# Kernel tuning notes

Measured on AMD Instinct MI355X. Metric: run time of the kernel, lower is better.

The kernel has to match this reference:

```python
import jax, jax.numpy as jnp
import numpy as np

# norse.LIFCell default parameters
DT = 1e-3
TAU_SYN_INV = 200.0   # 1 / 5e-3
TAU_MEM_INV = 100.0   # 1 / 1e-2
V_TH = 1.0
V_LEAK = 0.0
V_RESET = 0.0
ALPHA = 100.0         # SuperSpike surrogate slope

T, B, N_IN, N_HIDDEN, N_OUT = 16, 4096, 784, 256, 10


@jax.custom_vjp
def heaviside(x):
    return (x > 0).astype(x.dtype)

def _h_fwd(x):
    return heaviside(x), x

def _h_bwd(x, g):
    # SuperSpike surrogate: d/dx H(x) ~ 1 / (alpha*|x| + 1)^2
    return (g / (ALPHA * jnp.abs(x) + 1.0) ** 2,)

heaviside.defvjp(_h_fwd, _h_bwd)


def lif_step(inp, v, i):
    """One norse lif_step: Euler-integrate v and i, spike, hard reset."""
    v_decayed = v + DT * TAU_MEM_INV * ((V_LEAK - v) + i)
    i_decayed = i - DT * TAU_SYN_INV * i
    z = heaviside(v_decayed - V_TH)
    v_new = (1.0 - z) * v_decayed + z * V_RESET
    i_new = i_decayed + inp
    return z, v_new, i_new


def setup_inputs() -> dict:
    key = jax.random.key(0)
    k1, k2, k3, k4, k5 = jax.random.split(key, 5)
    # binary spike trains (T, B, N_IN)
    spike_input = (jax.random.uniform(k1, (T, B, N_IN)) < 0.3).astype(jnp.float32)
    lim1 = float(1.0 / np.sqrt(N_IN))
    lim2 = float(1.0 / np.sqrt(N_HIDDEN))
    W1 = jax.random.uniform(k2, (N_HIDDEN, N_IN), minval=-lim1, maxval=lim1, dtype=jnp.float32)
    b1 = jax.random.uniform(k3, (N_HIDDEN,), minval=-lim1, maxval=lim1, dtype=jnp.float32)
    W2 = jax.random.uniform(k4, (N_OUT, N_HIDDEN), minval=-lim2, maxval=lim2, dtype=jnp.float32)
    b2 = jax.random.uniform(k5, (N_OUT,), minval=-lim2, maxval=lim2, dtype=jnp.float32)
    return {"spike_input": spike_input, "W1": W1, "b1": b1, "W2": W2, "b2": b2}


def reference(spike_input, W1, b1, W2, b2):
    batch = spike_input.shape[1]
    nh, no = W1.shape[0], W2.shape[0]
    dtype = spike_input.dtype
    # LIFCell with state=None starts at v=v_leak, i=0
    init = (jnp.full((batch, nh), V_LEAK, dtype), jnp.zeros((batch, nh), dtype),
            jnp.full((batch, no), V_LEAK, dtype), jnp.zeros((batch, no), dtype))

    def step(carry, x_t):
        v1, i1, v2, i2 = carry
        c1 = x_t @ W1.T + b1                 # (B, N_HIDDEN)
        z1, v1, i1 = lif_step(c1, v1, i1)
        c2 = z1 @ W2.T + b2                  # (B, N_OUT)
        z2, v2, i2 = lif_step(c2, v2, i2)
        return (v1, i1, v2, i2), z2

    _, zs = jax.lax.scan(step, init, spike_input)  # zs: (T, B, N_OUT)
    return zs.sum(axis=0)                          # (B, N_OUT)
```

## Files before the change

kernel.cpp:

```cpp
#include <hip/hip_runtime.h>


#define T_STEPS 16
#define B_SZ    4096
#define N_IN    784
#define N_HID   256
#define N_OUT   10
#define M_TOT   (T_STEPS * B_SZ)
#define KP8     832
#define NSTEP   13
#define WPLANE  (N_HID * KP8)

typedef int    i32x4 __attribute__((ext_vector_type(4)));
typedef unsigned int u32;
typedef unsigned char u8;

#define GLOAD_LDS(SRC, DST) \
    __builtin_amdgcn_global_load_lds( \
        (const __attribute__((address_space(1))) void*)(SRC), \
        (__attribute__((address_space(3))) void*)(DST), 16, 0, 0)

__global__ __launch_bounds__(256) void conv_x(
    const float* __restrict__ X, u8* __restrict__ Xq)
{
    const long idx = (long)blockIdx.x * 256 + threadIdx.x;
    const long m = idx / 52;
    const int  s = (int)(idx - m * 52);
    uint4 o = make_uint4(0u, 0u, 0u, 0u);
    if (s < 49) {
        const uint4* src = reinterpret_cast<const uint4*>(X + m * N_IN + s * 16);
        const uint4 f0 = src[0], f1 = src[1], f2 = src[2], f3 = src[3];
        auto pk = [](uint4 f) -> u32 {
            return (f.x ? 1u : 0u) | ((f.y ? 1u : 0u) << 8) |
                   ((f.z ? 1u : 0u) << 16) | ((f.w ? 1u : 0u) << 24);
        };
        o.x = pk(f0); o.y = pk(f1); o.z = pk(f2); o.w = pk(f3);
    }
    reinterpret_cast<uint4*>(Xq)[idx] = o;
}

__global__ __launch_bounds__(256) void conv_w3(
    const float* __restrict__ W1, char* __restrict__ Wq)
{
    const int idx = blockIdx.x * 256 + threadIdx.x;
    if (idx >= N_HID * KP8) return;
    const int n = idx / KP8, k = idx % KP8;
    const float w = (k < N_IN) ? W1[n * N_IN + k] : 0.0f;
    const float a = rintf(w * 2048.0f);
    const float r1 = fmaf(a, -4.8828125e-4f, w);
    const float b = rintf(r1 * 262144.0f);
    const float r2 = fmaf(b, -3.814697265625e-6f, r1);
    const float c = rintf(r2 * 33554432.0f);
    Wq[idx]              = (char)(int)a;
    Wq[WPLANE + idx]     = (char)(int)b;
    Wq[2 * WPLANE + idx] = (char)(int)c;
}

__global__ __launch_bounds__(256, 2) void gemm1_i8(
    const u8* __restrict__ Xq,
    const u8* __restrict__ Wq,
    const float* __restrict__ b1,
    float* __restrict__ C)
{
    __shared__ u8 Bq[3 * 32 * KP8];

    const int tid  = threadIdx.x;
    const int lane = tid & 63;
    const int w    = tid >> 6;
    const int bid = blockIdx.x;
    const int mt  = (bid & 7) | ((bid >> 6) << 3);
    const int ns  = (bid >> 3) & 7;
    const int m0  = mt * 256;
    const int n0  = ns * 32;
    const int ls  = lane >> 4;
    const int lr  = lane & 15;

    {
        const int nIt = (w < 2) ? 20 : 19;
        for (int it = 0; it < nIt; ++it) {
            const int u     = it * 256 + tid;
            const int plane = u / 1664;
            const int rem   = u - plane * 1664;
            const int row   = rem / 52;
            const int sp    = rem - row * 52;
            const int sl    = (sp & ~3) | ((sp & 3) ^ (row & 3));
            const u8* src = Wq + (size_t)plane * WPLANE +
                            (size_t)(n0 + row) * KP8 + sl * 16;
            GLOAD_LDS(src, &Bq[u * 16]);
        }
    }
    __syncthreads();

    const u8* aP[4];
    #pragma unroll
    for (int i = 0; i < 4; ++i)
        aP[i] = Xq + (size_t)(m0 + w * 64 + i * 16 + lr) * KP8 + ls * 16;

    int bOff[2][3];
    #pragma unroll
    for (int j = 0; j < 2; ++j) {
        const int row = j * 16 + lr;
        #pragma unroll
        for (int p = 0; p < 3; ++p)
            bOff[j][p] = p * (32 * KP8) + row * KP8 + ((ls ^ (row & 3)) << 4);
    }

    i32x4 acc[4][2][3];
    #pragma unroll
    for (int i = 0; i < 4; ++i)
        #pragma unroll
        for (int j = 0; j < 2; ++j)
            #pragma unroll
            for (int p = 0; p < 3; ++p)
                acc[i][j][p] = (i32x4){0, 0, 0, 0};

    auto mmstep = [&](const uint4* af, int s) {
        uint4 bf[2][3];
        #pragma unroll
        for (int j = 0; j < 2; ++j)
            #pragma unroll
            for (int p = 0; p < 3; ++p)
                bf[j][p] = *reinterpret_cast<const uint4*>(&Bq[bOff[j][p] + s * 64]);
        #pragma unroll
        for (int i = 0; i < 4; ++i)
            #pragma unroll
            for (int j = 0; j < 2; ++j)
                #pragma unroll
                for (int p = 0; p < 3; ++p)
                    acc[i][j][p] = __builtin_amdgcn_mfma_i32_16x16x64_i8(
                        __builtin_bit_cast(i32x4, af[i]),
                        __builtin_bit_cast(i32x4, bf[j][p]),
                        acc[i][j][p], 0, 0, 0);
    };

    uint4 afA[4], afB[4];
    #pragma unroll
    for (int i = 0; i < 4; ++i)
        afA[i] = *reinterpret_cast<const uint4*>(aP[i]);

    for (int s = 0; s < 12; s += 2) {
        #pragma unroll
        for (int i = 0; i < 4; ++i)
            afB[i] = *reinterpret_cast<const uint4*>(aP[i] + (s + 1) * 64);
        mmstep(afA, s);
        #pragma unroll
        for (int i = 0; i < 4; ++i)
            afA[i] = *reinterpret_cast<const uint4*>(aP[i] + (s + 2) * 64);
        mmstep(afB, s + 1);
    }
    mmstep(afA, 12);

    const float s1 = 4.8828125e-4f;
    const float s2 = 3.814697265625e-6f;
    const float s3 = 2.9802322387695312e-8f;
    #pragma unroll
    for (int j = 0; j < 2; ++j) {
        const int col  = n0 + j * 16 + lr;
        const float bb = b1[col];
        #pragma unroll
        for (int i = 0; i < 4; ++i) {
            const int rbase = m0 + w * 64 + i * 16 + (ls << 2);
            #pragma unroll
            for (int q = 0; q < 4; ++q) {
                const float v = fmaf(s1, (float)acc[i][j][0][q],
                                fmaf(s2, (float)acc[i][j][1][q],
                                fmaf(s3, (float)acc[i][j][2][q], bb)));
                C[(size_t)(rbase + q) * N_HID + col] = v;
            }
        }
    }
}

__global__ __launch_bounds__(256) void lif1_kernel(float* __restrict__ C1)
{
    const int g = blockIdx.x * 256 + threadIdx.x;
    const size_t stride = (size_t)B_SZ * N_HID;
    float v = 0.0f, cur = 0.0f;
    #pragma unroll
    for (int t = 0; t < T_STEPS; ++t) {
        const size_t off = (size_t)t * stride + g;
        const float c = C1[off];
        const float vd = v + 0.1f * ((0.0f - v) + cur);
        const float id = cur - 0.2f * cur;
        const bool  sp = vd > 1.0f;
        C1[off] = sp ? 1.0f : 0.0f;
        v = sp ? 0.0f : vd;
        cur = id + c;
    }
}

__global__ __launch_bounds__(640) void gemm2_f32(
    const float* __restrict__ Z, const float* __restrict__ W2,
    const float* __restrict__ b2, float* __restrict__ C2)
{
    __shared__ float zs[64 * 268];
    __shared__ float ws[N_OUT * N_HID];
    const int tid = threadIdx.x;
    const int m0 = blockIdx.x * 64;

    for (int idx = tid; idx < 4096; idx += 640) {
        const int r = idx >> 6;
        const int c = (idx & 63) << 2;
        *(float4*)&zs[r * 268 + c] =
            *(const float4*)&Z[(size_t)(m0 + r) * N_HID + c];
    }
    *(float4*)&ws[tid * 4] = *(const float4*)&W2[tid * 4];
    __syncthreads();

    const int o = tid >> 6;
    const int r = tid & 63;
    float acc = b2[o];
    #pragma unroll
    for (int k = 0; k < N_HID; k += 4) {
        const float4 z4 = *(const float4*)&zs[r * 268 + k];
        const float4 w4 = *(const float4*)&ws[o * N_HID + k];
        acc += z4.x * w4.x + z4.y * w4.y + z4.z * w4.z + z4.w * w4.w;
    }
    C2[(size_t)(m0 + r) * N_OUT + o] = acc;
}

__global__ __launch_bounds__(256) void lif2_kernel(
    const float* __restrict__ C2, float* __restrict__ out)
{
    const int g = blockIdx.x * 256 + threadIdx.x;
    const int stride = B_SZ * N_OUT;
    float v = 0.0f, cur = 0.0f, s = 0.0f;
    #pragma unroll
    for (int t = 0; t < T_STEPS; ++t) {
        const float c = C2[t * stride + g];
        const float vd = v + 0.1f * ((0.0f - v) + cur);
        const float id = cur - 0.2f * cur;
        const bool  sp = vd > 1.0f;
        s += sp ? 1.0f : 0.0f;
        v = sp ? 0.0f : vd;
        cur = id + c;
    }
    out[g] = s;
}

extern "C" void kernel_launch(void* const* d_in, const int* in_sizes, int n_in,
                              void* d_out, int out_size, void* d_ws, size_t ws_size,
                              hipStream_t stream)
{
    const float* X  = (const float*)d_in[0];
    const float* W1 = (const float*)d_in[1];
    const float* b1 = (const float*)d_in[2];
    const float* W2 = (const float*)d_in[3];
    const float* b2 = (const float*)d_in[4];
    float* out = (float*)d_out;

    char* Wq = (char*)d_ws;
    u8*   Xq = (u8*)d_ws + (1 << 20);
    float* C1 = (float*)((char*)d_ws + (1 << 20) + (size_t)M_TOT * KP8);
    float* C2 = C1 + (size_t)M_TOT * N_HID;

    conv_x<<<(M_TOT * (KP8 / 16)) / 256, 256, 0, stream>>>(X, Xq);

    conv_w3<<<(N_HID * KP8) / 256, 256, 0, stream>>>(W1, Wq);

    gemm1_i8<<<2048, 256, 0, stream>>>(Xq, (const u8*)Wq, b1, C1);

    lif1_kernel<<<(B_SZ * N_HID) / 256, 256, 0, stream>>>(C1);

    gemm2_f32<<<M_TOT / 64, 640, 0, stream>>>(C1, W2, b2, C2);

    lif2_kernel<<<(B_SZ * N_OUT) / 256, 256, 0, stream>>>(C2, out);
}
```

Measured before the change: 143.1 us.

## Fuse layer-1 LIF into int8 GEMM epilogue and emit byte spikes

Restructures the first GEMM so each block owns 128 batch rows by 16 hidden units and loops over all 16 time steps. The LIF membrane state stays in registers and only spikes are written, as bytes. This removes the fp32 C1 round trip and the separate lif1 kernel, and gemm2 now reads the byte spikes. The cost is a smaller per-block tile with less MFMA reuse, a serial time loop inside each block, only 512 blocks, byte-granular scattered stores, and the W tile now staged through registers with padded rows instead of async global-to-LDS loads.

Result: faster. 131.1 us (-8.4%).

```diff
diff --git a/kernel.cpp b/kernel.cpp
--- a/kernel.cpp
+++ b/kernel.cpp
@@ -8,17 +8,13 @@
 #define N_OUT   10
 #define M_TOT   (T_STEPS * B_SZ)
 #define KP8     832
-#define NSTEP   13
 #define WPLANE  (N_HID * KP8)
+#define WROW    848
+#define WPL     (16 * WROW)
 
 typedef int    i32x4 __attribute__((ext_vector_type(4)));
 typedef unsigned int u32;
 typedef unsigned char u8;
-
-#define GLOAD_LDS(SRC, DST) \
-    __builtin_amdgcn_global_load_lds( \
-        (const __attribute__((address_space(1))) void*)(SRC), \
-        (__attribute__((address_space(3))) void*)(DST), 16, 0, 0)
 
 __global__ __launch_bounds__(256) void conv_x(
     const float* __restrict__ X, u8* __restrict__ Xq)
@@ -56,141 +52,112 @@
     Wq[2 * WPLANE + idx] = (char)(int)c;
 }
 
-__global__ __launch_bounds__(256, 2) void gemm1_i8(
+__global__ __launch_bounds__(256, 2) void gemm1_lif1(
     const u8* __restrict__ Xq,
     const u8* __restrict__ Wq,
     const float* __restrict__ b1,
-    float* __restrict__ C)
-{
-    __shared__ u8 Bq[3 * 32 * KP8];
+    u8* __restrict__ Z1)
+{
+    __shared__ u8 Bq[3 * WPL];
 
     const int tid  = threadIdx.x;
     const int lane = tid & 63;
     const int w    = tid >> 6;
     const int bid = blockIdx.x;
-    const int mt  = (bid & 7) | ((bid >> 6) << 3);
-    const int ns  = (bid >> 3) & 7;
-    const int m0  = mt * 256;
-    const int n0  = ns * 32;
+    const int l   = (bid & 7) * 64 + (bid >> 3);
+    const int b0  = (l >> 4) * 128;
+    const int n0  = (l & 15) * 16;
     const int ls  = lane >> 4;
     const int lr  = lane & 15;
 
-    {
-        const int nIt = (w < 2) ? 20 : 19;
-        for (int it = 0; it < nIt; ++it) {
-            const int u     = it * 256 + tid;
-            const int plane = u / 1664;
-            const int rem   = u - plane * 1664;
+    #pragma unroll
+    for (int it = 0; it < 10; ++it) {
+        const int u = it * 256 + tid;
+        if (u < 2496) {
+            const int plane = u / 832;
+            const int rem   = u - plane * 832;
             const int row   = rem / 52;
             const int sp    = rem - row * 52;
-            const int sl    = (sp & ~3) | ((sp & 3) ^ (row & 3));
-            const u8* src = Wq + (size_t)plane * WPLANE +
-                            (size_t)(n0 + row) * KP8 + sl * 16;
-            GLOAD_LDS(src, &Bq[u * 16]);
+            const uint4 v = *reinterpret_cast<const uint4*>(
+                Wq + (size_t)plane * WPLANE + (size_t)(n0 + row) * KP8 + sp * 16);
+            *reinterpret_cast<uint4*>(&Bq[plane * WPL + row * WROW + sp * 16]) = v;
         }
     }
     __syncthreads();
 
-    const u8* aP[4];
-    #pragma unroll
-    for (int i = 0; i < 4; ++i)
-        aP[i] = Xq + (size_t)(m0 + w * 64 + i * 16 + lr) * KP8 + ls * 16;
-
-    int bOff[2][3];
-    #pragma unroll
-    for (int j = 0; j < 2; ++j) {
-        const int row = j * 16 + lr;
-        #pragma unroll
-        for (int p = 0; p < 3; ++p)
-            bOff[j][p] = p * (32 * KP8) + row * KP8 + ((ls ^ (row & 3)) << 4);
-    }
-
-    i32x4 acc[4][2][3];
-    #pragma unroll
-    for (int i = 0; i < 4; ++i)
-        #pragma unroll
-        for (int j = 0; j < 2; ++j)
-            #pragma unroll
-            for (int p = 0; p < 3; ++p)
-                acc[i][j][p] = (i32x4){0, 0, 0, 0};
-
-    auto mmstep = [&](const uint4* af, int s) {
-        uint4 bf[2][3];
-        #pragma unroll
-        for (int j = 0; j < 2; ++j)
-            #pragma unroll
-            for (int p = 0; p < 3; ++p)
-                bf[j][p] = *reinterpret_cast<const uint4*>(&Bq[bOff[j][p] + s * 64]);
-        #pragma unroll
-        for (int i = 0; i < 4; ++i)
-            #pragma unroll
-            for (int j = 0; j < 2; ++j)
-                #pragma unroll
-                for (int p = 0; p < 3; ++p)
-                    acc[i][j][p] = __builtin_amdgcn_mfma_i32_16x16x64_i8(
-                        __builtin_bit_cast(i32x4, af[i]),
-                        __builtin_bit_cast(i32x4, bf[j][p]),
-                        acc[i][j][p], 0, 0, 0);
-    };
-
-    uint4 afA[4], afB[4];
-    #pragma unroll
-    for (int i = 0; i < 4; ++i)
-        afA[i] = *reinterpret_cast<const uint4*>(aP[i]);
-
-    for (int s = 0; s < 12; s += 2) {
-        #pragma unroll
-        for (int i = 0; i < 4; ++i)
-            afB[i] = *reinterpret_cast<const uint4*>(aP[i] + (s + 1) * 64);
-        mmstep(afA, s);
-        #pragma unroll
-        for (int i = 0; i < 4; ++i)
-            afA[i] = *reinterpret_cast<const uint4*>(aP[i] + (s + 2) * 64);
-        mmstep(afB, s + 1);
-    }
-    mmstep(afA, 12);
+    const float bb = b1[n0 + lr];
+    float vS[8], cS[8];
+    #pragma unroll
+    for (int k = 0; k < 8; ++k) { vS[k] = 0.0f; cS[k] = 0.0f; }
+
+    int bO[3];
+    #pragma unroll
+    for (int p = 0; p < 3; ++p) bO[p] = p * WPL + lr * WROW + (ls << 4);
+
+    const u8* aP0 = Xq + (size_t)(b0 + w * 32 + lr) * KP8 + ls * 16;
+    const u8* aP1 = aP0 + 16 * KP8;
+    const size_t TSTR = (size_t)B_SZ * KP8;
 
     const float s1 = 4.8828125e-4f;
     const float s2 = 3.814697265625e-6f;
     const float s3 = 2.9802322387695312e-8f;
-    #pragma unroll
-    for (int j = 0; j < 2; ++j) {
-        const int col  = n0 + j * 16 + lr;
-        const float bb = b1[col];
-        #pragma unroll
-        for (int i = 0; i < 4; ++i) {
-            const int rbase = m0 + w * 64 + i * 16 + (ls << 2);
+
+    for (int t = 0; t < T_STEPS; ++t) {
+        i32x4 acc[2][3];
+        #pragma unroll
+        for (int i = 0; i < 2; ++i)
+            #pragma unroll
+            for (int p = 0; p < 3; ++p)
+                acc[i][p] = (i32x4){0, 0, 0, 0};
+
+        uint4 ab[2][2];
+        ab[0][0] = *reinterpret_cast<const uint4*>(aP0);
+        ab[0][1] = *reinterpret_cast<const uint4*>(aP1);
+
+        #pragma unroll
+        for (int s = 0; s < 13; ++s) {
+            const int cb = s & 1;
+            if (s < 12) {
+                ab[cb ^ 1][0] = *reinterpret_cast<const uint4*>(aP0 + (s + 1) * 64);
+                ab[cb ^ 1][1] = *reinterpret_cast<const uint4*>(aP1 + (s + 1) * 64);
+            }
+            uint4 bf[3];
+            #pragma unroll
+            for (int p = 0; p < 3; ++p)
+                bf[p] = *reinterpret_cast<const uint4*>(&Bq[bO[p] + s * 64]);
+            #pragma unroll
+            for (int i = 0; i < 2; ++i)
+                #pragma unroll
+                for (int p = 0; p < 3; ++p)
+                    acc[i][p] = __builtin_amdgcn_mfma_i32_16x16x64_i8(
+                        __builtin_bit_cast(i32x4, ab[cb][i]),
+                        __builtin_bit_cast(i32x4, bf[p]),
+                        acc[i][p], 0, 0, 0);
+        }
+        aP0 += TSTR; aP1 += TSTR;
+
+        #pragma unroll
+        for (int i = 0; i < 2; ++i) {
             #pragma unroll
             for (int q = 0; q < 4; ++q) {
-                const float v = fmaf(s1, (float)acc[i][j][0][q],
-                                fmaf(s2, (float)acc[i][j][1][q],
-                                fmaf(s3, (float)acc[i][j][2][q], bb)));
-                C[(size_t)(rbase + q) * N_HID + col] = v;
+                const int k = i * 4 + q;
+                const float c1 = fmaf(s1, (float)acc[i][0][q],
+                                 fmaf(s2, (float)acc[i][1][q],
+                                 fmaf(s3, (float)acc[i][2][q], bb)));
+                const float vd = vS[k] + 0.1f * ((0.0f - vS[k]) + cS[k]);
+                const float id = cS[k] - 0.2f * cS[k];
+                const bool  sp = vd > 1.0f;
+                Z1[(size_t)(t * B_SZ + b0 + w * 32 + i * 16 + ls * 4 + q) * N_HID
+                   + n0 + lr] = sp ? (u8)1 : (u8)0;
+                vS[k] = sp ? 0.0f : vd;
+                cS[k] = id + c1;
             }
         }
     }
 }
 
-__global__ __launch_bounds__(256) void lif1_kernel(float* __restrict__ C1)
-{
-    const int g = blockIdx.x * 256 + threadIdx.x;
-    const size_t stride = (size_t)B_SZ * N_HID;
-    float v = 0.0f, cur = 0.0f;
-    #pragma unroll
-    for (int t = 0; t < T_STEPS; ++t) {
-        const size_t off = (size_t)t * stride + g;
-        const float c = C1[off];
-        const float vd = v + 0.1f * ((0.0f - v) + cur);
-        const float id = cur - 0.2f * cur;
-        const bool  sp = vd > 1.0f;
-        C1[off] = sp ? 1.0f : 0.0f;
-        v = sp ? 0.0f : vd;
-        cur = id + c;
-    }
-}
-
 __global__ __launch_bounds__(640) void gemm2_f32(
-    const float* __restrict__ Z, const float* __restrict__ W2,
+    const u8* __restrict__ Z, const float* __restrict__ W2,
     const float* __restrict__ b2, float* __restrict__ C2)
 {
     __shared__ float zs[64 * 268];
@@ -198,11 +165,18 @@
     const int tid = threadIdx.x;
     const int m0 = blockIdx.x * 64;
 
-    for (int idx = tid; idx < 4096; idx += 640) {
-        const int r = idx >> 6;
-        const int c = (idx & 63) << 2;
-        *(float4*)&zs[r * 268 + c] =
-            *(const float4*)&Z[(size_t)(m0 + r) * N_HID + c];
+    for (int c = tid; c < 1024; c += 640) {
+        const int r = c >> 4;
+        const int col = (c & 15) * 16;
+        const uint4 v = *reinterpret_cast<const uint4*>(
+            Z + (size_t)(m0 + r) * N_HID + col);
+        float* d = &zs[r * 268 + col];
+        const u32 wd[4] = {v.x, v.y, v.z, v.w};
+        #pragma unroll
+        for (int k = 0; k < 4; ++k)
+            #pragma unroll
+            for (int b = 0; b < 4; ++b)
+                d[k * 4 + b] = (float)((wd[k] >> (8 * b)) & 0xffu);
     }
     *(float4*)&ws[tid * 4] = *(const float4*)&W2[tid * 4];
     __syncthreads();
@@ -251,18 +225,16 @@
 
     char* Wq = (char*)d_ws;
     u8*   Xq = (u8*)d_ws + (1 << 20);
-    float* C1 = (float*)((char*)d_ws + (1 << 20) + (size_t)M_TOT * KP8);
-    float* C2 = C1 + (size_t)M_TOT * N_HID;
+    u8*   Z1 = Xq + (size_t)M_TOT * KP8;
+    float* C2 = (float*)(Z1 + (size_t)M_TOT * N_HID);
 
     conv_x<<<(M_TOT * (KP8 / 16)) / 256, 256, 0, stream>>>(X, Xq);
 
     conv_w3<<<(N_HID * KP8) / 256, 256, 0, stream>>>(W1, Wq);
 
-    gemm1_i8<<<2048, 256, 0, stream>>>(Xq, (const u8*)Wq, b1, C1);
-
-    lif1_kernel<<<(B_SZ * N_HID) / 256, 256, 0, stream>>>(C1);
-
-    gemm2_f32<<<M_TOT / 64, 640, 0, stream>>>(C1, W2, b2, C2);
+    gemm1_lif1<<<512, 256, 0, stream>>>(Xq, (const u8*)Wq, b1, Z1);
+
+    gemm2_f32<<<M_TOT / 64, 640, 0, stream>>>(Z1, W2, b2, C2);
 
     lif2_kernel<<<(B_SZ * N_OUT) / 256, 256, 0, stream>>>(C2, out);
 }
```
